# Kernel optimization log

Hardware: AMD Instinct MI355X
Metric: run time of the kernel (lower is better)

The kernel has to match this reference:

```python
import jax, jax.numpy as jnp
import numpy as np

B, S, D, C, I = 2, 1024, 1024, 64, 2048
N = S // C            # num_chunks (S divisible by C -> no padding)
EPS = 1e-6
BASE_LR = 0.01


def setup_inputs() -> dict:
    key = jax.random.key(0)
    ks = jax.random.split(key, 12)
    def xavier(k, shape):
        fan_in = shape[-1]
        return jax.random.normal(k, shape, jnp.float32) * (1.0 / np.sqrt(fan_in))
    return {
        "x": jax.random.normal(ks[0], (B, S, D), jnp.float32),
        "w1": xavier(ks[1], (I, D)),          # memory layer 0 weight [out,in]
        "w2": xavier(ks[2], (D, I)),          # memory layer 1 weight
        "ln_w": jnp.ones((D,), jnp.float32),  # memory RMSNorm weight
        "wq": xavier(ks[3], (D, D)),
        "wk": xavier(ks[4], (D, D)),
        "wv": xavier(ks[5], (D, D)),
        "qn_w": jnp.ones((D,), jnp.float32),
        "kn_w": jnp.ones((D,), jnp.float32),
        "alpha_w": jax.random.normal(ks[6], (1, C * D), jnp.float32) * 1e-3,
        "theta_w": jax.random.normal(ks[7], (1, C * D), jnp.float32) * 1e-3,
        "eta_w": jax.random.normal(ks[8], (1, C * D), jnp.float32) * 1e-3,
    }


def _rms(x, w):
    return x * jax.lax.rsqrt(jnp.mean(x * x, axis=-1, keepdims=True) + EPS) * w


def _memory_fwd(params, x):
    # 2-layer MLP memory with RMSNorm + residual
    w1, w2, lnw = params
    h = jax.nn.silu(x @ w1.T)
    y = h @ w2.T
    return x + _rms(y, lnw)


def _comb(e1, e2):
    # binary_operator: (a_j*a_i, kv_j + a_j*kv_i)
    a_i, kv_i = e1
    a_j, kv_j = e2
    return (a_j * a_i, kv_j + a_j * kv_i)


def _assocscan_update(pm, ps, g, eta, alpha):
    # pm,ps: [B,*s], g: [B,N,*s], eta/alpha: [B,N]
    extra = g.ndim - 2
    e = eta.reshape(eta.shape + (1,) * extra)
    a = alpha.reshape(alpha.shape + (1,) * extra)
    ones = jnp.ones_like(e[:, :1])
    # surprise recurrence: S_t = eta_t * S_{t-1} - g_t
    cS = jnp.concatenate([ones, e], axis=1)
    vS = jnp.concatenate([ps[:, None], -g], axis=1)
    _, Ssec = jax.lax.associative_scan(_comb, (cS, vS), axis=1)
    # memory recurrence: M_t = (1-alpha_t) * M_{t-1} + S_t
    cM = jnp.concatenate([ones, 1.0 - a], axis=1)
    vM = jnp.concatenate([pm[:, None], Ssec[:, 1:]], axis=1)
    _, Msec = jax.lax.associative_scan(_comb, (cM, vM), axis=1)
    return Msec[:, -1], Ssec[:, -1]


def reference(x, w1, w2, ln_w, wq, wk, wv, qn_w, kn_w, alpha_w, theta_w, eta_w):
    x4 = x.reshape(B, N, C, D)
    xc = x4.reshape(B, N, C * D)
    alpha = jax.nn.sigmoid(xc @ alpha_w.T)[..., 0]           # [B,N]
    theta = jax.nn.sigmoid(xc @ theta_w.T) * BASE_LR         # [B,N,1]
    eta = jax.nn.sigmoid(xc @ eta_w.T)[..., 0]               # [B,N]

    k = _rms(jax.nn.silu(x4 @ wk.T), kn_w)                   # [B,N,C,D]
    v = jax.nn.silu(x4 @ wv.T)                               # [B,N,C,D]

    # batched memory params (get_memory_params expands over batch)
    bw1 = jnp.broadcast_to(w1, (B,) + w1.shape)
    bw2 = jnp.broadcast_to(w2, (B,) + w2.shape)
    bln = jnp.broadcast_to(ln_w, (B,) + ln_w.shape)
    # initial surprises = 0
    s1 = jnp.zeros_like(bw1)
    s2 = jnp.zeros_like(bw2)
    sl = jnp.zeros_like(bln)

    def loss(p, ki, vi, th):
        pred = _memory_fwd(p, ki)
        return jnp.sum(jnp.mean((vi - pred) ** 2 * th, axis=-1))

    per_sample_grad = jax.vmap(jax.vmap(jax.grad(loss), in_axes=(None, 0, 0, 0)),
                               in_axes=(0, 0, 0, 0))
    g1, g2, gl = per_sample_grad((bw1, bw2, bln), k, v, theta)  # [B,N,*param]

    nw1, ns1 = _assocscan_update(bw1, s1, g1, eta, alpha)
    nw2, ns2 = _assocscan_update(bw2, s2, g2, eta, alpha)
    nln, nsl = _assocscan_update(bln, sl, gl, eta, alpha)

    # retrieve with updated memory
    q = _rms(jax.nn.silu(x4 @ wq.T), qn_w)                   # [B,N,C,D]
    out = jax.vmap(_memory_fwd)((nw1, nw2, nln), q)          # [B,N,C,D]
    out = out.reshape(B, S, D)
    return (out, nw1, nw2, nln, ns1, ns2, nsl)
```

## Files before the change

kernel.cpp:

```cpp
#include <hip/hip_runtime.h>

#define KD 1024
#define KI 2048
#define KB 2
#define KS 1024
#define KC 64
#define KN 16
#define KEPS 1e-6f

typedef __bf16 bf16x8 __attribute__((ext_vector_type(8)));
typedef __bf16 bf16x4 __attribute__((ext_vector_type(4)));
typedef float f32x4 __attribute__((ext_vector_type(4)));

__device__ __forceinline__ float sigf(float x){ return 1.0f/(1.0f+__expf(-x)); }
__device__ __forceinline__ float siluf(float x){ return x*sigf(x); }
__device__ __forceinline__ float dsiluf(float x){ float s=sigf(x); return s*(1.0f+x*(1.0f-s)); }

__device__ __forceinline__ void gld16(const __bf16* g, __bf16* l) {
  __builtin_amdgcn_global_load_lds(
    (const __attribute__((address_space(1))) unsigned int*)g,
    (__attribute__((address_space(3))) unsigned int*)l, 16, 0, 0);
}

template<int SRCF>
__device__ __forceinline__ void tconv_body(const void* in, __bf16* out,
                                           int R, int Cc, int bx, int by)
{
  __shared__ float T[64][65];
  const int r0 = by*64, c0 = bx*64;
  const int tx = threadIdx.x & 15, ty = threadIdx.x >> 4;
  #pragma unroll
  for (int i=0;i<4;i++){
    const int r = r0 + ty + i*16;
    if (SRCF) {
      const float4 v = *(const float4*)((const float*)in + (size_t)r*Cc + c0 + tx*4);
      T[ty+i*16][tx*4+0]=v.x; T[ty+i*16][tx*4+1]=v.y;
      T[ty+i*16][tx*4+2]=v.z; T[ty+i*16][tx*4+3]=v.w;
    } else {
      const bf16x4 v = *(const bf16x4*)((const __bf16*)in + (size_t)r*Cc + c0 + tx*4);
      T[ty+i*16][tx*4+0]=(float)v[0]; T[ty+i*16][tx*4+1]=(float)v[1];
      T[ty+i*16][tx*4+2]=(float)v[2]; T[ty+i*16][tx*4+3]=(float)v[3];
    }
  }
  __syncthreads();
  #pragma unroll
  for (int i=0;i<4;i++){
    bf16x4 o = { (__bf16)T[tx*4+0][ty+i*16], (__bf16)T[tx*4+1][ty+i*16],
                 (__bf16)T[tx*4+2][ty+i*16], (__bf16)T[tx*4+3][ty+i*16] };
    *(bf16x4*)(out + (size_t)(c0+ty+i*16)*R + r0 + tx*4) = o;
  }
}

__global__ __launch_bounds__(256) void prep_kernel(
  const float* __restrict__ x, const float* __restrict__ wk, const float* __restrict__ wv,
  const float* __restrict__ wq, const float* __restrict__ w1, const float* __restrict__ w2,
  const float* __restrict__ aw, const float* __restrict__ tw, const float* __restrict__ ew,
  __bf16* __restrict__ xb, __bf16* __restrict__ wkb, __bf16* __restrict__ wvb,
  __bf16* __restrict__ wqb, __bf16* __restrict__ w1b, __bf16* __restrict__ w2b,
  __bf16* __restrict__ w2tb, float* __restrict__ part, float* __restrict__ gl)
{
  const int g = blockIdx.x;
  if (g < 9216) {
    const long t = (long)g*256 + threadIdx.x;
    const float* s; __bf16* d; long i;
    if (t < 524288)       { s=x;  d=xb;  i=t; }
    else if (t < 786432)  { s=wk; d=wkb; i=t-524288; }
    else if (t < 1048576) { s=wv; d=wvb; i=t-786432; }
    else if (t < 1310720) { s=wq; d=wqb; i=t-1048576; }
    else if (t < 1835008) { s=w1; d=w1b; i=t-1310720; }
    else                  { s=w2; d=w2b; i=t-1835008; }
    const float4 v = *(const float4*)(s + i*4);
    bf16x4 o = { (__bf16)v.x, (__bf16)v.y, (__bf16)v.z, (__bf16)v.w };
    *(bf16x4*)(d + i*4) = o;
  } else if (g < 9728) {
    const int gg = g - 9216;
    const int seg = gg & 15, bn = gg >> 4;
    const int base = seg*4096;
    float da=0.f, dt=0.f, de=0.f;
    #pragma unroll
    for (int i=0;i<4;i++){
      const int off = base + i*1024 + threadIdx.x*4;
      const float4 xv = *(const float4*)(x + (size_t)bn*65536 + off);
      const float4 av = *(const float4*)(aw + off);
      const float4 tv = *(const float4*)(tw + off);
      const float4 ev = *(const float4*)(ew + off);
      da += xv.x*av.x + xv.y*av.y + xv.z*av.z + xv.w*av.w;
      dt += xv.x*tv.x + xv.y*tv.y + xv.z*tv.z + xv.w*tv.w;
      de += xv.x*ev.x + xv.y*ev.y + xv.z*ev.z + xv.w*ev.w;
    }
    __shared__ float sA[256], sT[256], sE[256];
    sA[threadIdx.x]=da; sT[threadIdx.x]=dt; sE[threadIdx.x]=de;
    __syncthreads();
    for (int s=128;s>0;s>>=1){
      if ((int)threadIdx.x < s){
        sA[threadIdx.x]+=sA[threadIdx.x+s];
        sT[threadIdx.x]+=sT[threadIdx.x+s];
        sE[threadIdx.x]+=sE[threadIdx.x+s];
      }
      __syncthreads();
    }
    if (threadIdx.x==0){
      part[0*512 + bn*16 + seg] = sA[0];
      part[1*512 + bn*16 + seg] = sT[0];
      part[2*512 + bn*16 + seg] = sE[0];
    }
  } else if (g < 10240) {
    const int gg = g - 9728;
    tconv_body<1>(w2, w2tb, 1024, 2048, gg & 31, gg >> 5);
  } else {
    const int gg = g - 10240;
    float4 z = {0.f,0.f,0.f,0.f};
    *(float4*)(gl + (size_t)gg*1024 + threadIdx.x*4) = z;
  }
}

__global__ void scan_coef_kernel(const float* __restrict__ part,
                                 float* __restrict__ cm, float* __restrict__ cs,
                                 float* __restrict__ Pw, float* __restrict__ theta)
{
  const int b = threadIdx.x;
  if (b >= KB) return;
  float al[KN], et[KN];
  for (int n=0;n<KN;n++){
    float sa=0.f, st=0.f, se=0.f;
    for (int s=0;s<16;s++){
      sa += part[0*512 + (b*KN+n)*16 + s];
      st += part[1*512 + (b*KN+n)*16 + s];
      se += part[2*512 + (b*KN+n)*16 + s];
    }
    al[n] = sigf(sa);
    theta[b*KN+n] = sigf(st)*0.01f;
    et[n] = sigf(se);
  }
  float prodE = 1.f;
  for (int j=KN-1;j>=0;j--){ cs[b*KN+j] = -prodE; prodE *= et[j]; }
  float A[KN]; A[KN-1]=1.f;
  for (int t=KN-2;t>=0;t--) A[t] = A[t+1]*(1.f-al[t+1]);
  for (int j=0;j<KN;j++){
    float inner=0.f, E=1.f;
    for (int t=j;t<KN;t++){ inner += A[t]*E; if (t+1<KN) E *= et[t+1]; }
    cm[b*KN+j] = -inner;
  }
  float pw=1.f;
  for (int n=0;n<KN;n++) pw *= (1.f-al[n]);
  Pw[b]=pw;
}

template<int EPI, int MODE>
__global__ __launch_bounds__(256) void mgemm2(
    const __bf16* __restrict__ A, const __bf16* __restrict__ B0,
    const __bf16* __restrict__ B1, const __bf16* __restrict__ B2,
    float* __restrict__ F0, float* __restrict__ F1,
    __bf16* __restrict__ Oa, __bf16* __restrict__ Ob, const __bf16* __restrict__ Aux,
    int M, int Nn, int lda, int ldb, long bstr)
{
  const int bz = blockIdx.z;
  const int n0 = blockIdx.x * 64;
  const int m0 = blockIdx.y * 128;
  const __bf16* Bp = B0;
  if (MODE==1) { if (bz==1) Bp=B1; else if (bz==2) Bp=B2; }
  float* F0p = F0;
  int koff0 = 0;
  if (MODE==2) { koff0 = bz << 10; F0p = F0 + (size_t)bz * M * Nn; }
  Bp += (size_t)(m0 >> 10) * (size_t)bstr;
  __shared__ __bf16 As[2*128*64];
  __shared__ __bf16 Bs[2*64*64];
  const int tid = threadIdx.x, wv = tid >> 6, lane = tid & 63;
  const int wm = (wv >> 1) << 6, wn = (wv & 1) << 5;
  const int fr = lane & 15, fg = lane >> 4;
  const int lr = lane >> 3, lc = lane & 7;
  const __bf16* asrc[4]; __bf16* adst[4];
  const __bf16* bsrc[2]; __bf16* bdst[2];
  #pragma unroll
  for (int i=0;i<4;i++){
    const int rowbase=(wv*4+i)*8, row=rowbase+lr;
    asrc[i] = A + (size_t)(m0+row)*lda + koff0 + ((lc^(row&7))<<3);
    adst[i] = As + rowbase*64;
  }
  #pragma unroll
  for (int i=0;i<2;i++){
    const int rowbase=(wv*2+i)*8, row=rowbase+lr;
    bsrc[i] = Bp + (size_t)(n0+row)*ldb + koff0 + ((lc^(row&7))<<3);
    bdst[i] = Bs + rowbase*64;
  }
  f32x4 acc[4][2] = {};
  #pragma unroll
  for (int i=0;i<4;i++) gld16(asrc[i], adst[i]);
  #pragma unroll
  for (int i=0;i<2;i++) gld16(bsrc[i], bdst[i]);
  __syncthreads();
  #pragma unroll 2
  for (int t=0;t<16;++t){
    const int p = t & 1;
    if (t < 15){
      const int ko = (t+1) << 6;
      const int q = p ^ 1;
      #pragma unroll
      for (int i=0;i<4;i++) gld16(asrc[i]+ko, adst[i]+q*8192);
      #pragma unroll
      for (int i=0;i<2;i++) gld16(bsrc[i]+ko, bdst[i]+q*4096);
    }
    #pragma unroll
    for (int ks=0;ks<2;++ks){
      bf16x8 af[4], bfv[2];
      #pragma unroll
      for (int mi=0;mi<4;++mi){
        const int r = wm + mi*16 + fr;
        af[mi] = *(const bf16x8*)(As + p*8192 + r*64 + ((((ks<<2)+fg)^(r&7))<<3));
      }
      #pragma unroll
      for (int ni=0;ni<2;++ni){
        const int r = wn + ni*16 + fr;
        bfv[ni] = *(const bf16x8*)(Bs + p*4096 + r*64 + ((((ks<<2)+fg)^(r&7))<<3));
      }
      #pragma unroll
      for (int mi=0;mi<4;++mi)
        #pragma unroll
        for (int ni=0;ni<2;++ni)
          acc[mi][ni] = __builtin_amdgcn_mfma_f32_16x16x32_bf16(af[mi], bfv[ni], acc[mi][ni], 0,0,0);
    }
    __syncthreads();
  }
  #pragma unroll
  for (int mi=0;mi<4;++mi){
    #pragma unroll
    for (int ni=0;ni<2;++ni){
      #pragma unroll
      for (int j=0;j<4;++j){
        const int m = m0 + wm + mi*16 + fg*4 + j;
        const int n = n0 + wn + ni*16 + fr;
        const size_t idx = (size_t)m * Nn + n;
        const float v = acc[mi][ni][j];
        if (EPI==0) F0p[idx] = v;
        else if (EPI==2) { Oa[idx] = (__bf16)siluf(v); Ob[idx] = (__bf16)dsiluf(v); }
        else if (EPI==3) Oa[idx] = (__bf16)(v * (float)Aux[idx]);
        else if (EPI==4) Oa[idx] = (__bf16)siluf(v);
        else if (EPI==5) {
          if (bz==0) F0[idx] = siluf(v);
          else if (bz==1) Oa[idx] = (__bf16)siluf(v);
          else F1[idx] = siluf(v);
        }
      }
    }
  }
}

__global__ __launch_bounds__(256) void wacc2k_kernel(
    const __bf16* __restrict__ A, const __bf16* __restrict__ B,
    const float* __restrict__ Winit,
    const float* __restrict__ cm, const float* __restrict__ cs,
    const float* __restrict__ Pw,
    float* __restrict__ outM, __bf16* __restrict__ outMb, float* __restrict__ outS,
    int M, int Nn, int lda, int ldb)
{
  const int bz = blockIdx.z;
  const int n0 = blockIdx.x * 64;
  const int m0 = blockIdx.y * 128;
  const int koff0 = bz << 10;
  __shared__ __bf16 As[2*128*64];
  __shared__ __bf16 Bs[2*64*64];
  const int tid = threadIdx.x, wv = tid >> 6, lane = tid & 63;
  const int wm = (wv >> 1) << 6, wn = (wv & 1) << 5;
  const int fr = lane & 15, fg = lane >> 4;
  const int lr = lane >> 3, lc = lane & 7;
  const __bf16* asrc[4]; __bf16* adst[4];
  const __bf16* bsrc[2]; __bf16* bdst[2];
  #pragma unroll
  for (int i=0;i<4;i++){
    const int rowbase=(wv*4+i)*8, row=rowbase+lr;
    asrc[i] = A + (size_t)(m0+row)*lda + koff0 + ((lc^(row&7))<<3);
    adst[i] = As + rowbase*64;
  }
  #pragma unroll
  for (int i=0;i<2;i++){
    const int rowbase=(wv*2+i)*8, row=rowbase+lr;
    bsrc[i] = B + (size_t)(n0+row)*ldb + koff0 + ((lc^(row&7))<<3);
    bdst[i] = Bs + rowbase*64;
  }
  f32x4 accM[4][2] = {}, accS[4][2] = {};
  #pragma unroll
  for (int i=0;i<4;i++) gld16(asrc[i], adst[i]);
  #pragma unroll
  for (int i=0;i<2;i++) gld16(bsrc[i], bdst[i]);
  __syncthreads();
  #pragma unroll 2
  for (int t=0;t<16;++t){
    const int p = t & 1;
    const float cmc = cm[bz*KN + t], csc = cs[bz*KN + t];
    if (t < 15){
      const int ko = (t+1) << 6;
      const int q = p ^ 1;
      #pragma unroll
      for (int i=0;i<4;i++) gld16(asrc[i]+ko, adst[i]+q*8192);
      #pragma unroll
      for (int i=0;i<2;i++) gld16(bsrc[i]+ko, bdst[i]+q*4096);
    }
    bf16x8 a0[4], a1[4], b0[2], b1[2];
    #pragma unroll
    for (int mi=0;mi<4;++mi){
      const int r = wm + mi*16 + fr;
      a0[mi] = *(const bf16x8*)(As + p*8192 + r*64 + (((0+fg)^(r&7))<<3));
      a1[mi] = *(const bf16x8*)(As + p*8192 + r*64 + (((4+fg)^(r&7))<<3));
    }
    #pragma unroll
    for (int ni=0;ni<2;++ni){
      const int r = wn + ni*16 + fr;
      b0[ni] = *(const bf16x8*)(Bs + p*4096 + r*64 + (((0+fg)^(r&7))<<3));
      b1[ni] = *(const bf16x8*)(Bs + p*4096 + r*64 + (((4+fg)^(r&7))<<3));
    }
    #pragma unroll
    for (int mi=0;mi<4;++mi){
      #pragma unroll
      for (int ni=0;ni<2;++ni){
        const f32x4 zf = {0.f,0.f,0.f,0.f};
        f32x4 P = __builtin_amdgcn_mfma_f32_16x16x32_bf16(a0[mi], b0[ni], zf, 0,0,0);
        P = __builtin_amdgcn_mfma_f32_16x16x32_bf16(a1[mi], b1[ni], P, 0,0,0);
        accM[mi][ni] += P * cmc;
        accS[mi][ni] += P * csc;
      }
    }
    __syncthreads();
  }
  const float pw = Pw[bz];
  #pragma unroll
  for (int mi=0;mi<4;++mi){
    #pragma unroll
    for (int ni=0;ni<2;++ni){
      #pragma unroll
      for (int j=0;j<4;++j){
        const int m = m0 + wm + mi*16 + fg*4 + j;
        const int n = n0 + wn + ni*16 + fr;
        const size_t widx = (size_t)m * Nn + n;
        const size_t oidx = (size_t)bz * M * Nn + widx;
        const float vm = pw * Winit[widx] + accM[mi][ni][j];
        outM[oidx] = vm;
        outMb[oidx] = (__bf16)vm;
        outS[oidx] = accS[mi][ni][j];
      }
    }
  }
}

__global__ __launch_bounds__(256) void rmsfuse_kernel(
    const float* __restrict__ kv, const float* __restrict__ kw, __bf16* __restrict__ k16,
    const float* __restrict__ qv, const float* __restrict__ qw, __bf16* __restrict__ q16)
{
  const float* v; const float* w; __bf16* o16;
  if (blockIdx.y == 0){ v=kv; w=kw; o16=k16; } else { v=qv; w=qw; o16=q16; }
  const int row = blockIdx.x * 4 + (threadIdx.x >> 6);
  const int lane = threadIdx.x & 63;
  const float* p = v + (size_t)row * KD;
  __bf16* p16 = o16 + (size_t)row * KD;
  float vals[16]; float ss = 0.f;
  #pragma unroll
  for (int l=0;l<16;l++){ vals[l] = p[lane + (l<<6)]; ss += vals[l]*vals[l]; }
  #pragma unroll
  for (int o=32;o>0;o>>=1) ss += __shfl_xor(ss, o, 64);
  const float inv = rsqrtf(ss * (1.0f/KD) + KEPS);
  #pragma unroll
  for (int l=0;l<16;l++){
    const int d = lane + (l<<6);
    p16[d] = (__bf16)(vals[l]*inv*w[d]);
  }
}

__global__ __launch_bounds__(256) void rms_grad_kernel(
    const float* __restrict__ y0, const float* __restrict__ y1,
    const __bf16* __restrict__ k16, const __bf16* __restrict__ v16,
    const float* __restrict__ lnw, const float* __restrict__ theta,
    __bf16* __restrict__ gy, float* __restrict__ gl)
{
  const int wv = threadIdx.x >> 6;
  const int row = blockIdx.x * 4 + wv;
  const int lane = threadIdx.x & 63;
  const int chunk = blockIdx.x >> 4;
  const float th2 = theta[chunk] * (2.0f / KD);
  const float* yr0 = y0 + (size_t)row * KD;
  const float* yr1 = y1 + (size_t)row * KD;
  const __bf16* kr = k16 + (size_t)row * KD;
  const __bf16* vr = v16 + (size_t)row * KD;
  float yv[16]; float ss = 0.f;
  #pragma unroll
  for (int l=0;l<16;l++){
    const int d = lane + (l<<6);
    yv[l] = yr0[d] + yr1[d]; ss += yv[l]*yv[l];
  }
  #pragma unroll
  for (int o=32;o>0;o>>=1) ss += __shfl_xor(ss, o, 64);
  const float inv = rsqrtf(ss * (1.0f/KD) + KEPS);
  float gzv[16]; float sdot = 0.f;
  #pragma unroll
  for (int l=0;l<16;l++){
    const int d = lane + (l<<6);
    const float gz = th2 * ((float)kr[d] + yv[l]*inv*lnw[d] - (float)vr[d]);
    gzv[l] = gz;
    sdot += gz * lnw[d] * yv[l];
  }
  #pragma unroll
  for (int o=32;o>0;o>>=1) sdot += __shfl_xor(sdot, o, 64);
  const float c3 = inv*inv*inv * (1.0f/KD) * sdot;
  __bf16* gyr = gy + (size_t)row * KD;
  __shared__ float L[4][KD];
  #pragma unroll
  for (int l=0;l<16;l++){
    const int d = lane + (l<<6);
    gyr[d] = (__bf16)(inv * lnw[d] * gzv[l] - c3 * yv[l]);
    L[wv][d] = gzv[l] * yv[l] * inv;
  }
  __syncthreads();
  if (wv == 0){
    float* glc = gl + (size_t)chunk * KD;
    #pragma unroll
    for (int l=0;l<16;l++){
      const int d = lane + (l<<6);
      atomicAdd(&glc[d], L[0][d]+L[1][d]+L[2][d]+L[3][d]);
    }
  }
}

__global__ __launch_bounds__(256) void tconv4_kernel(
    const __bf16* __restrict__ kb16, __bf16* __restrict__ kT,
    const __bf16* __restrict__ hb16, __bf16* __restrict__ hT,
    const __bf16* __restrict__ gyb,  __bf16* __restrict__ gyT,
    const __bf16* __restrict__ gab,  __bf16* __restrict__ gaT)
{
  const int g = blockIdx.x;
  if (g < 512)        tconv_body<0>(kb16, kT, 2048, 1024, g & 15, g >> 4);
  else if (g < 1536){ const int t = g - 512;  tconv_body<0>(hb16, hT, 2048, 2048, t & 31, t >> 5); }
  else if (g < 2048){ const int t = g - 1536; tconv_body<0>(gyb, gyT, 2048, 1024, t & 15, t >> 4); }
  else              { const int t = g - 2048; tconv_body<0>(gab, gaT, 2048, 2048, t & 31, t >> 5); }
}

__global__ void glcomb_kernel(const float* __restrict__ gl, const float* __restrict__ lnw,
                              const float* __restrict__ cm, const float* __restrict__ cs,
                              const float* __restrict__ Pw,
                              float* __restrict__ nln, float* __restrict__ nsl)
{
  const int idx = blockIdx.x*256 + threadIdx.x;
  const int b = idx >> 10, d = idx & (KD-1);
  float am=0.f, as=0.f;
  for (int n=0;n<KN;n++){
    const float g = gl[(size_t)(b*KN+n)*KD + d];
    am += cm[b*KN+n]*g; as += cs[b*KN+n]*g;
  }
  nln[idx] = Pw[b]*lnw[d] + am;
  nsl[idx] = as;
}

__global__ __launch_bounds__(256) void final_out_kernel(
    const __bf16* __restrict__ q16, const float* __restrict__ yq0,
    const float* __restrict__ yq1, const float* __restrict__ nln,
    float* __restrict__ out)
{
  const int row = blockIdx.x * 4 + (threadIdx.x >> 6);
  const int lane = threadIdx.x & 63;
  const int b = row >> 10;
  float yv[16]; float ss = 0.f;
  #pragma unroll
  for (int l=0;l<16;l++){
    const int d = lane + (l<<6);
    yv[l] = yq0[(size_t)row*KD + d] + yq1[(size_t)row*KD + d];
    ss += yv[l]*yv[l];
  }
  #pragma unroll
  for (int o=32;o>0;o>>=1) ss += __shfl_xor(ss, o, 64);
  const float inv = rsqrtf(ss * (1.0f/KD) + KEPS);
  #pragma unroll
  for (int l=0;l<16;l++){
    const int d = lane + (l<<6);
    out[(size_t)row*KD + d] = (float)q16[(size_t)row*KD + d] + yv[l]*inv*nln[b*KD + d];
  }
}

extern "C" void kernel_launch(void* const* d_in, const int* in_sizes, int n_in,
                              void* d_out, int out_size, void* d_ws, size_t ws_size,
                              hipStream_t stream)
{
  const float* x    = (const float*)d_in[0];
  const float* w1   = (const float*)d_in[1];
  const float* w2   = (const float*)d_in[2];
  const float* lnw  = (const float*)d_in[3];
  const float* wq   = (const float*)d_in[4];
  const float* wk   = (const float*)d_in[5];
  const float* wv   = (const float*)d_in[6];
  const float* qnw  = (const float*)d_in[7];
  const float* knw  = (const float*)d_in[8];
  const float* aw   = (const float*)d_in[9];
  const float* tw   = (const float*)d_in[10];
  const float* ew   = (const float*)d_in[11];

  float* out = (float*)d_out;
  float* nw1 = out + (size_t)KB*KS*KD;
  float* nw2 = nw1 + (size_t)KB*KI*KD;
  float* nln = nw2 + (size_t)KB*KD*KI;
  float* ns1 = nln + (size_t)KB*KD;
  float* ns2 = ns1 + (size_t)KB*KI*KD;
  float* nsl = ns2 + (size_t)KB*KD*KI;

  float* ws = (float*)d_ws;
  size_t o = 0;
  float* kbuf = ws+o; o += 2097152;
  float* qbuf = ws+o; o += 2097152;
  float* ybuf = ws+o; o += 2097152;
  float* ybuf2= ws+o; o += 2097152;
  float* gl   = ws+o; o += 32768;
  float* part = ws+o; o += 1536;
  float* cmb  = ws+o; o += 32;
  float* csb  = ws+o; o += 32;
  float* Pwb  = ws+o; o += 32;
  float* thetab = ws+o; o += 32;
  __bf16* bb = (__bf16*)(ws + o);
  size_t p = 0;
  __bf16* xb   = bb+p; p += 2097152;
  __bf16* wkb  = bb+p; p += 1048576;
  __bf16* wvb  = bb+p; p += 1048576;
  __bf16* wqb  = bb+p; p += 1048576;
  __bf16* w1b  = bb+p; p += 2097152;
  __bf16* w2b  = bb+p; p += 2097152;
  __bf16* w2tb = bb+p; p += 2097152;
  __bf16* kb16 = bb+p; p += 2097152;
  __bf16* qb16 = bb+p; p += 2097152;
  __bf16* vb16 = bb+p; p += 2097152;
  __bf16* hb16 = bb+p; p += 4194304;
  __bf16* db16 = bb+p; p += 4194304;
  __bf16* gab  = bb+p; p += 4194304;
  __bf16* hT   = bb+p; p += 4194304;
  __bf16* nw1b = bb+p; p += 4194304;
  __bf16* nw2b = bb+p; p += 4194304;
  __bf16* gyT = xb;
  __bf16* kT  = wkb;
  __bf16* gyb = w1b;
  __bf16* gaT = w2b;
  __bf16* hq16= gab;

  dim3 blk(256);

  prep_kernel<<<10272, blk, 0, stream>>>(x, wk, wv, wq, w1, w2, aw, tw, ew,
      xb, wkb, wvb, wqb, w1b, w2b, w2tb, part, gl);
  scan_coef_kernel<<<1, 64, 0, stream>>>(part, cmb, csb, Pwb, thetab);

  mgemm2<5,1><<<dim3(16,16,3), blk, 0, stream>>>(xb, wkb, wvb, wqb,
      kbuf, qbuf, vb16, nullptr, nullptr, 2048, 1024, 1024, 1024, 0);
  rmsfuse_kernel<<<dim3(512,2), blk, 0, stream>>>(kbuf, knw, kb16, qbuf, qnw, qb16);

  mgemm2<2,0><<<dim3(32,16,1), blk, 0, stream>>>(kb16, w1b, nullptr, nullptr,
      nullptr, nullptr, hb16, db16, nullptr, 2048, 2048, 1024, 1024, 0);
  mgemm2<0,2><<<dim3(16,16,2), blk, 0, stream>>>(hb16, w2b, nullptr, nullptr,
      ybuf, nullptr, nullptr, nullptr, nullptr, 2048, 1024, 2048, 2048, 0);
  rms_grad_kernel<<<512, blk, 0, stream>>>(ybuf, ybuf2, kb16, vb16, lnw, thetab, gyb, gl);
  mgemm2<3,0><<<dim3(32,16,1), blk, 0, stream>>>(gyb, w2tb, nullptr, nullptr,
      nullptr, nullptr, gab, nullptr, db16, 2048, 2048, 1024, 1024, 0);
  tconv4_kernel<<<3072, blk, 0, stream>>>(kb16, kT, hb16, hT, gyb, gyT, gab, gaT);

  wacc2k_kernel<<<dim3(16,16,2), blk, 0, stream>>>(gaT, kT, w1, cmb, csb, Pwb,
      nw1, nw1b, ns1, 2048, 1024, 2048, 2048);
  wacc2k_kernel<<<dim3(32,8,2), blk, 0, stream>>>(gyT, hT, w2, cmb, csb, Pwb,
      nw2, nw2b, ns2, 1024, 2048, 2048, 2048);
  glcomb_kernel<<<8, blk, 0, stream>>>(gl, lnw, cmb, csb, Pwb, nln, nsl);

  mgemm2<4,0><<<dim3(32,16,1), blk, 0, stream>>>(qb16, nw1b, nullptr, nullptr,
      nullptr, nullptr, hq16, nullptr, nullptr, 2048, 2048, 1024, 1024, (long)KI*KD);
  mgemm2<0,2><<<dim3(16,16,2), blk, 0, stream>>>(hq16, nw2b, nullptr, nullptr,
      ybuf, nullptr, nullptr, nullptr, nullptr, 2048, 1024, 2048, 2048, (long)KD*KI);
  final_out_kernel<<<512, blk, 0, stream>>>(qb16, ybuf, ybuf2, nln, out);
}
```

Before: 230.1 us.

## Fuse transposes into GEMM epilogues, merge small kernels, store split-K partials as bf16

The GEMM epilogue can now write a transposed bf16 copy through LDS, so the separate transpose passes for h and ga go away. The gate dot-products move into the x conversion blocks, and the scan-coefficient computation is folded into the RMS kernel. The two weight-accumulate GEMMs and the ln-weight combine are merged into one launch. Split-K partial outputs are stored as bf16 instead of fp32, which halves that traffic but loses precision in the y sums.

Result: faster. 211.4 us (-8.1%).

```diff
diff --git a/kernel.cpp b/kernel.cpp
--- a/kernel.cpp
+++ b/kernel.cpp
@@ -60,11 +60,36 @@
   __bf16* __restrict__ w2tb, float* __restrict__ part, float* __restrict__ gl)
 {
   const int g = blockIdx.x;
-  if (g < 9216) {
+  if (g < 2048) {
+    const int i = g*256 + threadIdx.x;
+    const float4 xv = *(const float4*)(x + (size_t)i*4);
+    bf16x4 o = { (__bf16)xv.x, (__bf16)xv.y, (__bf16)xv.z, (__bf16)xv.w };
+    *(bf16x4*)(xb + (size_t)i*4) = o;
+    const size_t co = (size_t)(i & 16383) * 4;
+    const float4 av = *(const float4*)(aw + co);
+    const float4 tv = *(const float4*)(tw + co);
+    const float4 ev = *(const float4*)(ew + co);
+    float da = xv.x*av.x + xv.y*av.y + xv.z*av.z + xv.w*av.w;
+    float dt = xv.x*tv.x + xv.y*tv.y + xv.z*tv.z + xv.w*tv.w;
+    float de = xv.x*ev.x + xv.y*ev.y + xv.z*ev.z + xv.w*ev.w;
+    __shared__ float sA[256], sT[256], sE[256];
+    sA[threadIdx.x]=da; sT[threadIdx.x]=dt; sE[threadIdx.x]=de;
+    __syncthreads();
+    for (int s=128;s>0;s>>=1){
+      if ((int)threadIdx.x < s){
+        sA[threadIdx.x]+=sA[threadIdx.x+s];
+        sT[threadIdx.x]+=sT[threadIdx.x+s];
+        sE[threadIdx.x]+=sE[threadIdx.x+s];
+      }
+      __syncthreads();
+    }
+    if (threadIdx.x==0){
+      part[g] = sA[0]; part[2048+g] = sT[0]; part[4096+g] = sE[0];
+    }
+  } else if (g < 9216) {
     const long t = (long)g*256 + threadIdx.x;
     const float* s; __bf16* d; long i;
-    if (t < 524288)       { s=x;  d=xb;  i=t; }
-    else if (t < 786432)  { s=wk; d=wkb; i=t-524288; }
+    if (t < 786432)       { s=wk; d=wkb; i=t-524288; }
     else if (t < 1048576) { s=wv; d=wvb; i=t-786432; }
     else if (t < 1310720) { s=wq; d=wqb; i=t-1048576; }
     else if (t < 1835008) { s=w1; d=w1b; i=t-1310720; }
@@ -74,84 +99,21 @@
     *(bf16x4*)(d + i*4) = o;
   } else if (g < 9728) {
     const int gg = g - 9216;
-    const int seg = gg & 15, bn = gg >> 4;
-    const int base = seg*4096;
-    float da=0.f, dt=0.f, de=0.f;
-    #pragma unroll
-    for (int i=0;i<4;i++){
-      const int off = base + i*1024 + threadIdx.x*4;
-      const float4 xv = *(const float4*)(x + (size_t)bn*65536 + off);
-      const float4 av = *(const float4*)(aw + off);
-      const float4 tv = *(const float4*)(tw + off);
-      const float4 ev = *(const float4*)(ew + off);
-      da += xv.x*av.x + xv.y*av.y + xv.z*av.z + xv.w*av.w;
-      dt += xv.x*tv.x + xv.y*tv.y + xv.z*tv.z + xv.w*tv.w;
-      de += xv.x*ev.x + xv.y*ev.y + xv.z*ev.z + xv.w*ev.w;
-    }
-    __shared__ float sA[256], sT[256], sE[256];
-    sA[threadIdx.x]=da; sT[threadIdx.x]=dt; sE[threadIdx.x]=de;
-    __syncthreads();
-    for (int s=128;s>0;s>>=1){
-      if ((int)threadIdx.x < s){
-        sA[threadIdx.x]+=sA[threadIdx.x+s];
-        sT[threadIdx.x]+=sT[threadIdx.x+s];
-        sE[threadIdx.x]+=sE[threadIdx.x+s];
-      }
-      __syncthreads();
-    }
-    if (threadIdx.x==0){
-      part[0*512 + bn*16 + seg] = sA[0];
-      part[1*512 + bn*16 + seg] = sT[0];
-      part[2*512 + bn*16 + seg] = sE[0];
-    }
-  } else if (g < 10240) {
-    const int gg = g - 9728;
     tconv_body<1>(w2, w2tb, 1024, 2048, gg & 31, gg >> 5);
   } else {
-    const int gg = g - 10240;
+    const int gg = g - 9728;
     float4 z = {0.f,0.f,0.f,0.f};
     *(float4*)(gl + (size_t)gg*1024 + threadIdx.x*4) = z;
   }
 }
 
-__global__ void scan_coef_kernel(const float* __restrict__ part,
-                                 float* __restrict__ cm, float* __restrict__ cs,
-                                 float* __restrict__ Pw, float* __restrict__ theta)
-{
-  const int b = threadIdx.x;
-  if (b >= KB) return;
-  float al[KN], et[KN];
-  for (int n=0;n<KN;n++){
-    float sa=0.f, st=0.f, se=0.f;
-    for (int s=0;s<16;s++){
-      sa += part[0*512 + (b*KN+n)*16 + s];
-      st += part[1*512 + (b*KN+n)*16 + s];
-      se += part[2*512 + (b*KN+n)*16 + s];
-    }
-    al[n] = sigf(sa);
-    theta[b*KN+n] = sigf(st)*0.01f;
-    et[n] = sigf(se);
-  }
-  float prodE = 1.f;
-  for (int j=KN-1;j>=0;j--){ cs[b*KN+j] = -prodE; prodE *= et[j]; }
-  float A[KN]; A[KN-1]=1.f;
-  for (int t=KN-2;t>=0;t--) A[t] = A[t+1]*(1.f-al[t+1]);
-  for (int j=0;j<KN;j++){
-    float inner=0.f, E=1.f;
-    for (int t=j;t<KN;t++){ inner += A[t]*E; if (t+1<KN) E *= et[t+1]; }
-    cm[b*KN+j] = -inner;
-  }
-  float pw=1.f;
-  for (int n=0;n<KN;n++) pw *= (1.f-al[n]);
-  Pw[b]=pw;
-}
-
-template<int EPI, int MODE>
+template<int EPI, int MODE, int WT>
 __global__ __launch_bounds__(256) void mgemm2(
     const __bf16* __restrict__ A, const __bf16* __restrict__ B0,
     const __bf16* __restrict__ B1, const __bf16* __restrict__ B2,
     float* __restrict__ F0, float* __restrict__ F1,
     __bf16* __restrict__ Oa, __bf16* __restrict__ Ob, const __bf16* __restrict__ Aux,
+    __bf16* __restrict__ OT, int ldt,
     int M, int Nn, int lda, int ldb, long bstr)
 {
   const int bz = blockIdx.z;
@@ -161,7 +123,7 @@
   if (MODE==1) { if (bz==1) Bp=B1; else if (bz==2) Bp=B2; }
   float* F0p = F0;
   int koff0 = 0;
-  if (MODE==2) { koff0 = bz << 10; F0p = F0 + (size_t)bz * M * Nn; }
+  if (MODE==2) { koff0 = bz << 10; }
   Bp += (size_t)(m0 >> 10) * (size_t)bstr;
   __shared__ __bf16 As[2*128*64];
   __shared__ __bf16 Bs[2*64*64];
@@ -221,44 +183,60 @@
     }
     __syncthreads();
   }
+  __bf16* T = As;
   #pragma unroll
   for (int mi=0;mi<4;++mi){
     #pragma unroll
     for (int ni=0;ni<2;++ni){
+      bf16x4 tv;
       #pragma unroll
       for (int j=0;j<4;++j){
         const int m = m0 + wm + mi*16 + fg*4 + j;
         const int n = n0 + wn + ni*16 + fr;
         const size_t idx = (size_t)m * Nn + n;
         const float v = acc[mi][ni][j];
+        float tval = 0.f;
         if (EPI==0) F0p[idx] = v;
-        else if (EPI==2) { Oa[idx] = (__bf16)siluf(v); Ob[idx] = (__bf16)dsiluf(v); }
-        else if (EPI==3) Oa[idx] = (__bf16)(v * (float)Aux[idx]);
+        else if (EPI==2) { const float sv = siluf(v); Oa[idx]=(__bf16)sv; Ob[idx]=(__bf16)dsiluf(v); tval=sv; }
+        else if (EPI==3) tval = v * (float)Aux[idx];
         else if (EPI==4) Oa[idx] = (__bf16)siluf(v);
         else if (EPI==5) {
           if (bz==0) F0[idx] = siluf(v);
           else if (bz==1) Oa[idx] = (__bf16)siluf(v);
           else F1[idx] = siluf(v);
         }
-      }
-    }
-  }
-}
-
-__global__ __launch_bounds__(256) void wacc2k_kernel(
+        else if (EPI==6) Oa[(size_t)bz*M*Nn + idx] = (__bf16)v;
+        if (WT) tv[j] = (__bf16)tval;
+      }
+      if (WT){
+        const int nl = wn + ni*16 + fr;
+        const int ml = wm + mi*16 + fg*4;
+        *(bf16x4*)(T + nl*128 + (ml ^ ((nl&7)<<3))) = tv;
+      }
+    }
+  }
+  if (WT){
+    __syncthreads();
+    const int tn = tid >> 2, tc = tid & 3;
+    #pragma unroll
+    for (int u=0;u<4;++u){
+      const int m8 = tc*32 + u*8;
+      const bf16x8 v = *(const bf16x8*)(T + tn*128 + (m8 ^ ((tn&7)<<3)));
+      *(bf16x8*)(OT + (size_t)(n0+tn)*ldt + m0 + m8) = v;
+    }
+  }
+}
+
+__device__ __forceinline__ void wacc_body(
+    __bf16* As, __bf16* Bs,
     const __bf16* __restrict__ A, const __bf16* __restrict__ B,
     const float* __restrict__ Winit,
     const float* __restrict__ cm, const float* __restrict__ cs,
     const float* __restrict__ Pw,
     float* __restrict__ outM, __bf16* __restrict__ outMb, float* __restrict__ outS,
-    int M, int Nn, int lda, int ldb)
-{
-  const int bz = blockIdx.z;
-  const int n0 = blockIdx.x * 64;
-  const int m0 = blockIdx.y * 128;
+    int M, int Nn, int lda, int ldb, int n0, int m0, int bz)
+{
   const int koff0 = bz << 10;
-  __shared__ __bf16 As[2*128*64];
-  __shared__ __bf16 Bs[2*64*64];
   const int tid = threadIdx.x, wv = tid >> 6, lane = tid & 63;
   const int wm = (wv >> 1) << 6, wn = (wv & 1) << 5;
   const int fr = lane & 15, fg = lane >> 4;
@@ -341,10 +319,83 @@
   }
 }
 
+__global__ __launch_bounds__(256) void waccall_kernel(
+    const __bf16* __restrict__ gaT, const __bf16* __restrict__ kT, const float* __restrict__ w1,
+    const __bf16* __restrict__ gyT, const __bf16* __restrict__ hT, const float* __restrict__ w2,
+    const float* __restrict__ gl, const float* __restrict__ lnw,
+    const float* __restrict__ cm, const float* __restrict__ cs, const float* __restrict__ Pw,
+    float* __restrict__ nw1, __bf16* __restrict__ nw1b, float* __restrict__ ns1,
+    float* __restrict__ nw2, __bf16* __restrict__ nw2b, float* __restrict__ ns2,
+    float* __restrict__ nln, float* __restrict__ nsl)
+{
+  __shared__ __bf16 As[2*128*64];
+  __shared__ __bf16 Bs[2*64*64];
+  const int g = blockIdx.x;
+  if (g < 512){
+    const int bz = g >> 8, rem = g & 255;
+    wacc_body(As, Bs, gaT, kT, w1, cm, cs, Pw, nw1, nw1b, ns1,
+              2048, 1024, 2048, 2048, (rem & 15)*64, (rem >> 4)*128, bz);
+  } else if (g < 1024){
+    const int t = g - 512;
+    const int bz = t >> 8, rem = t & 255;
+    wacc_body(As, Bs, gyT, hT, w2, cm, cs, Pw, nw2, nw2b, ns2,
+              1024, 2048, 2048, 2048, (rem & 31)*64, (rem >> 5)*128, bz);
+  } else {
+    const int idx = (g - 1024)*256 + threadIdx.x;
+    const int b = idx >> 10, d = idx & (KD-1);
+    float am=0.f, as=0.f;
+    for (int n=0;n<KN;n++){
+      const float gv = gl[(size_t)(b*KN+n)*KD + d];
+      am += cm[b*KN+n]*gv; as += cs[b*KN+n]*gv;
+    }
+    nln[idx] = Pw[b]*lnw[d] + am;
+    nsl[idx] = as;
+  }
+}
+
 __global__ __launch_bounds__(256) void rmsfuse_kernel(
     const float* __restrict__ kv, const float* __restrict__ kw, __bf16* __restrict__ k16,
-    const float* __restrict__ qv, const float* __restrict__ qw, __bf16* __restrict__ q16)
-{
+    const float* __restrict__ qv, const float* __restrict__ qw, __bf16* __restrict__ q16,
+    const float* __restrict__ part, float* __restrict__ cm, float* __restrict__ cs,
+    float* __restrict__ Pw, float* __restrict__ theta)
+{
+  if (blockIdx.y == 2){
+    if (blockIdx.x != 0) return;
+    __shared__ float P[32][8][3];
+    const int bn = threadIdx.x >> 3, sg = threadIdx.x & 7;
+    float s0=0.f, s1=0.f, s2=0.f;
+    #pragma unroll
+    for (int u=0;u<8;u++){
+      const int seg = bn*64 + sg*8 + u;
+      s0 += part[seg]; s1 += part[2048+seg]; s2 += part[4096+seg];
+    }
+    P[bn][sg][0]=s0; P[bn][sg][1]=s1; P[bn][sg][2]=s2;
+    __syncthreads();
+    if ((int)threadIdx.x < KB){
+      const int b = threadIdx.x;
+      float al[KN], et[KN];
+      for (int n=0;n<KN;n++){
+        const int c = b*KN+n;
+        float sa=0.f, st=0.f, se=0.f;
+        #pragma unroll
+        for (int k=0;k<8;k++){ sa+=P[c][k][0]; st+=P[c][k][1]; se+=P[c][k][2]; }
+        al[n]=sigf(sa); theta[c]=sigf(st)*0.01f; et[n]=sigf(se);
+      }
+      float prodE = 1.f;
+      for (int j=KN-1;j>=0;j--){ cs[b*KN+j] = -prodE; prodE *= et[j]; }
+      float Ac[KN]; Ac[KN-1]=1.f;
+      for (int t=KN-2;t>=0;t--) Ac[t] = Ac[t+1]*(1.f-al[t+1]);
+      for (int j=0;j<KN;j++){
+        float inner=0.f, E=1.f;
+        for (int t=j;t<KN;t++){ inner += Ac[t]*E; if (t+1<KN) E *= et[t+1]; }
+        cm[b*KN+j] = -inner;
+      }
+      float pw=1.f;
+      for (int n=0;n<KN;n++) pw *= (1.f-al[n]);
+      Pw[b]=pw;
+    }
+    return;
+  }
   const float* v; const float* w; __bf16* o16;
   if (blockIdx.y == 0){ v=kv; w=kw; o16=k16; } else { v=qv; w=qw; o16=q16; }
   const int row = blockIdx.x * 4 + (threadIdx.x >> 6);
@@ -365,7 +416,7 @@
 }
 
 __global__ __launch_bounds__(256) void rms_grad_kernel(
-    const float* __restrict__ y0, const float* __restrict__ y1,
+    const __bf16* __restrict__ y16,
     const __bf16* __restrict__ k16, const __bf16* __restrict__ v16,
     const float* __restrict__ lnw, const float* __restrict__ theta,
     __bf16* __restrict__ gy, float* __restrict__ gl)
@@ -375,15 +426,15 @@
   const int lane = threadIdx.x & 63;
   const int chunk = blockIdx.x >> 4;
   const float th2 = theta[chunk] * (2.0f / KD);
-  const float* yr0 = y0 + (size_t)row * KD;
-  const float* yr1 = y1 + (size_t)row * KD;
+  const __bf16* yr0 = y16 + (size_t)row * KD;
+  const __bf16* yr1 = y16 + 2097152 + (size_t)row * KD;
   const __bf16* kr = k16 + (size_t)row * KD;
   const __bf16* vr = v16 + (size_t)row * KD;
   float yv[16]; float ss = 0.f;
   #pragma unroll
   for (int l=0;l<16;l++){
     const int d = lane + (l<<6);
-    yv[l] = yr0[d] + yr1[d]; ss += yv[l]*yv[l];
+    yv[l] = (float)yr0[d] + (float)yr1[d]; ss += yv[l]*yv[l];
   }
   #pragma unroll
   for (int o=32;o>0;o>>=1) ss += __shfl_xor(ss, o, 64);
@@ -418,39 +469,18 @@
   }
 }
 
-__global__ __launch_bounds__(256) void tconv4_kernel(
+__global__ __launch_bounds__(256) void tconv2_kernel(
     const __bf16* __restrict__ kb16, __bf16* __restrict__ kT,
-    const __bf16* __restrict__ hb16, __bf16* __restrict__ hT,
-    const __bf16* __restrict__ gyb,  __bf16* __restrict__ gyT,
-    const __bf16* __restrict__ gab,  __bf16* __restrict__ gaT)
+    const __bf16* __restrict__ gyb,  __bf16* __restrict__ gyT)
 {
   const int g = blockIdx.x;
-  if (g < 512)        tconv_body<0>(kb16, kT, 2048, 1024, g & 15, g >> 4);
-  else if (g < 1536){ const int t = g - 512;  tconv_body<0>(hb16, hT, 2048, 2048, t & 31, t >> 5); }
-  else if (g < 2048){ const int t = g - 1536; tconv_body<0>(gyb, gyT, 2048, 1024, t & 15, t >> 4); }
-  else              { const int t = g - 2048; tconv_body<0>(gab, gaT, 2048, 2048, t & 31, t >> 5); }
-}
-
-__global__ void glcomb_kernel(const float* __restrict__ gl, const float* __restrict__ lnw,
-                              const float* __restrict__ cm, const float* __restrict__ cs,
-                              const float* __restrict__ Pw,
-                              float* __restrict__ nln, float* __restrict__ nsl)
-{
-  const int idx = blockIdx.x*256 + threadIdx.x;
-  const int b = idx >> 10, d = idx & (KD-1);
-  float am=0.f, as=0.f;
-  for (int n=0;n<KN;n++){
-    const float g = gl[(size_t)(b*KN+n)*KD + d];
-    am += cm[b*KN+n]*g; as += cs[b*KN+n]*g;
-  }
-  nln[idx] = Pw[b]*lnw[d] + am;
-  nsl[idx] = as;
+  if (g < 512)  tconv_body<0>(kb16, kT, 2048, 1024, g & 15, g >> 4);
+  else        { const int t = g - 512; tconv_body<0>(gyb, gyT, 2048, 1024, t & 15, t >> 4); }
 }
 
 __global__ __launch_bounds__(256) void final_out_kernel(
-    const __bf16* __restrict__ q16, const float* __restrict__ yq0,
-    const float* __restrict__ yq1, const float* __restrict__ nln,
-    float* __restrict__ out)
+    const __bf16* __restrict__ q16, const __bf16* __restrict__ yq16,
+    const float* __restrict__ nln, float* __restrict__ out)
 {
   const int row = blockIdx.x * 4 + (threadIdx.x >> 6);
   const int lane = threadIdx.x & 63;
@@ -459,7 +489,7 @@
   #pragma unroll
   for (int l=0;l<16;l++){
     const int d = lane + (l<<6);
-    yv[l] = yq0[(size_t)row*KD + d] + yq1[(size_t)row*KD + d];
+    yv[l] = (float)yq16[(size_t)row*KD + d] + (float)yq16[2097152 + (size_t)row*KD + d];
     ss += yv[l]*yv[l];
   }
   #pragma unroll
@@ -501,10 +531,8 @@
   size_t o = 0;
   float* kbuf = ws+o; o += 2097152;
   float* qbuf = ws+o; o += 2097152;
-  float* ybuf = ws+o; o += 2097152;
-  float* ybuf2= ws+o; o += 2097152;
   float* gl   = ws+o; o += 32768;
-  float* part = ws+o; o += 1536;
+  float* part = ws+o; o += 6144;
   float* cmb  = ws+o; o += 32;
   float* csb  = ws+o; o += 32;
   float* Pwb  = ws+o; o += 32;
@@ -523,44 +551,37 @@
   __bf16* vb16 = bb+p; p += 2097152;
   __bf16* hb16 = bb+p; p += 4194304;
   __bf16* db16 = bb+p; p += 4194304;
-  __bf16* gab  = bb+p; p += 4194304;
   __bf16* hT   = bb+p; p += 4194304;
+  __bf16* gaT  = bb+p; p += 4194304;
   __bf16* nw1b = bb+p; p += 4194304;
   __bf16* nw2b = bb+p; p += 4194304;
+  __bf16* y16  = bb+p; p += 4194304;
   __bf16* gyT = xb;
   __bf16* kT  = wkb;
   __bf16* gyb = w1b;
-  __bf16* gaT = w2b;
-  __bf16* hq16= gab;
+  __bf16* hq16= w2b;
 
   dim3 blk(256);
 
-  prep_kernel<<<10272, blk, 0, stream>>>(x, wk, wv, wq, w1, w2, aw, tw, ew,
+  prep_kernel<<<9760, blk, 0, stream>>>(x, wk, wv, wq, w1, w2, aw, tw, ew,
       xb, wkb, wvb, wqb, w1b, w2b, w2tb, part, gl);
-  scan_coef_kernel<<<1, 64, 0, stream>>>(part, cmb, csb, Pwb, thetab);
-
-  mgemm2<5,1><<<dim3(16,16,3), blk, 0, stream>>>(xb, wkb, wvb, wqb,
-      kbuf, qbuf, vb16, nullptr, nullptr, 2048, 1024, 1024, 1024, 0);
-  rmsfuse_kernel<<<dim3(512,2), blk, 0, stream>>>(kbuf, knw, kb16, qbuf, qnw, qb16);
-
-  mgemm2<2,0><<<dim3(32,16,1), blk, 0, stream>>>(kb16, w1b, nullptr, nullptr,
-      nullptr, nullptr, hb16, db16, nullptr, 2048, 2048, 1024, 1024, 0);
-  mgemm2<0,2><<<dim3(16,16,2), blk, 0, stream>>>(hb16, w2b, nullptr, nullptr,
-      ybuf, nullptr, nullptr, nullptr, nullptr, 2048, 1024, 2048, 2048, 0);
-  rms_grad_kernel<<<512, blk, 0, stream>>>(ybuf, ybuf2, kb16, vb16, lnw, thetab, gyb, gl);
-  mgemm2<3,0><<<dim3(32,16,1), blk, 0, stream>>>(gyb, w2tb, nullptr, nullptr,
-      nullptr, nullptr, gab, nullptr, db16, 2048, 2048, 1024, 1024, 0);
-  tconv4_kernel<<<3072, blk, 0, stream>>>(kb16, kT, hb16, hT, gyb, gyT, gab, gaT);
-
-  wacc2k_kernel<<<dim3(16,16,2), blk, 0, stream>>>(gaT, kT, w1, cmb, csb, Pwb,
-      nw1, nw1b, ns1, 2048, 1024, 2048, 2048);
-  wacc2k_kernel<<<dim3(32,8,2), blk, 0, stream>>>(gyT, hT, w2, cmb, csb, Pwb,
-      nw2, nw2b, ns2, 1024, 2048, 2048, 2048);
-  glcomb_kernel<<<8, blk, 0, stream>>>(gl, lnw, cmb, csb, Pwb, nln, nsl);
-
-  mgemm2<4,0><<<dim3(32,16,1), blk, 0, stream>>>(qb16, nw1b, nullptr, nullptr,
-      nullptr, nullptr, hq16, nullptr, nullptr, 2048, 2048, 1024, 1024, (long)KI*KD);
-  mgemm2<0,2><<<dim3(16,16,2), blk, 0, stream>>>(hq16, nw2b, nullptr, nullptr,
-      ybuf, nullptr, nullptr, nullptr, nullptr, 2048, 1024, 2048, 2048, (long)KD*KI);
-  final_out_kernel<<<512, blk, 0, stream>>>(qb16, ybuf, ybuf2, nln, out);
-}
+  mgemm2<5,1,0><<<dim3(16,16,3), blk, 0, stream>>>(xb, wkb, wvb, wqb,
+      kbuf, qbuf, vb16, nullptr, nullptr, nullptr, 0, 2048, 1024, 1024, 1024, 0);
+  rmsfuse_kernel<<<dim3(512,3), blk, 0, stream>>>(kbuf, knw, kb16, qbuf, qnw, qb16,
+      part, cmb, csb, Pwb, thetab);
+  mgemm2<2,0,1><<<dim3(32,16,1), blk, 0, stream>>>(kb16, w1b, nullptr, nullptr,
+      nullptr, nullptr, hb16, db16, nullptr, hT, 2048, 2048, 2048, 1024, 1024, 0);
+  mgemm2<6,2,0><<<dim3(16,16,2), blk, 0, stream>>>(hb16, w2b, nullptr, nullptr,
+      nullptr, nullptr, y16, nullptr, nullptr, nullptr, 0, 2048, 1024, 2048, 2048, 0);
+  rms_grad_kernel<<<512, blk, 0, stream>>>(y16, kb16, vb16, lnw, thetab, gyb, gl);
+  tconv2_kernel<<<1024, blk, 0, stream>>>(kb16, kT, gyb, gyT);
+  mgemm2<3,0,1><<<dim3(32,16,1), blk, 0, stream>>>(gyb, w2tb, nullptr, nullptr,
+      nullptr, nullptr, nullptr, nullptr, db16, gaT, 2048, 2048, 2048, 1024, 1024, 0);
+  waccall_kernel<<<1032, blk, 0, stream>>>(gaT, kT, w1, gyT, hT, w2, gl, lnw,
+      cmb, csb, Pwb, nw1, nw1b, ns1, nw2, nw2b, ns2, nln, nsl);
+  mgemm2<4,0,0><<<dim3(32,16,1), blk, 0, stream>>>(qb16, nw1b, nullptr, nullptr,
+      nullptr, nullptr, hq16, nullptr, nullptr, nullptr, 0, 2048, 2048, 1024, 1024, (long)KI*KD);
+  mgemm2<6,2,0><<<dim3(16,16,2), blk, 0, stream>>>(hq16, nw2b, nullptr, nullptr,
+      nullptr, nullptr, y16, nullptr, nullptr, nullptr, 0, 2048, 1024, 2048, 2048, (long)KD*KI);
+  final_out_kernel<<<512, blk, 0, stream>>>(qb16, y16, nln, out);
+}
```
